# Optimization experiments

Hardware: AMD Instinct MI355X
Metric: run time of the kernel (lower is better)

## Reference

```python
import jax, jax.numpy as jnp
import numpy as np

N, M, K, C = 1000, 2000, 10, 80
IOU_THRESHOLD = 0.5
EPS = 1e-7


def setup_inputs() -> dict:
    key = jax.random.key(0)
    k1, k2, k3, k4, k5, k6, k7 = jax.random.split(key, 7)
    # pred boxes: realistic xyxy boxes in a 1000x1000 image
    cxy = jax.random.uniform(k1, (N, 2), minval=0.0, maxval=1000.0)
    wh = jax.random.uniform(k2, (N, 2), minval=20.0, maxval=100.0)
    pred_box = jnp.concatenate([cxy - wh / 2, cxy + wh / 2], axis=1)  # [N,4]
    pred = jnp.concatenate([pred_box, jax.random.uniform(k3, (N, 2))], axis=1)  # [N,6]
    # dropout passes: jittered copies of pred boxes (guarantees IoU>0.5 match)
    # followed by M-N random boxes
    copies = pred_box[None, :, :] + jax.random.normal(k4, (K, N, 4)) * 1.0  # [K,N,4]
    rc = jax.random.uniform(k5, (K, M - N, 2), minval=0.0, maxval=1000.0)
    rwh = jax.random.uniform(k6, (K, M - N, 2), minval=20.0, maxval=100.0)
    rand_box = jnp.concatenate([rc - rwh / 2, rc + rwh / 2], axis=2)  # [K,M-N,4]
    boxes = jnp.concatenate([copies, rand_box], axis=1)  # [K,M,4]
    dropout_preds = jnp.concatenate([boxes, jnp.ones((K, M, 2), jnp.float32)], axis=2)
    # per-box class probability rows (softmax-normalized, strictly positive)
    dropout_cls_confs = jax.nn.softmax(jax.random.normal(k7, (K, M, C)), axis=-1)
    return {
        "pred": pred.astype(jnp.float32),
        "dropout_preds": dropout_preds.astype(jnp.float32),
        "dropout_cls_confs": dropout_cls_confs.astype(jnp.float32),
    }


def _pairwise_iou(b1, b2):
    # b1: [N,4] xyxy, b2: [K,M,4] xyxy -> iou [K,N,M]
    ix1 = jnp.maximum(b1[None, :, None, 0], b2[:, None, :, 0])
    iy1 = jnp.maximum(b1[None, :, None, 1], b2[:, None, :, 1])
    ix2 = jnp.minimum(b1[None, :, None, 2], b2[:, None, :, 2])
    iy2 = jnp.minimum(b1[None, :, None, 3], b2[:, None, :, 3])
    inter = jnp.clip(ix2 - ix1, 0.0) * jnp.clip(iy2 - iy1, 0.0)  # [K,N,M]
    area1 = (b1[:, 2] - b1[:, 0]) * (b1[:, 3] - b1[:, 1])  # [N]
    area2 = (b2[..., 2] - b2[..., 0]) * (b2[..., 3] - b2[..., 1])  # [K,M]
    return inter / (area1[None, :, None] + area2[:, None, :] - inter + EPS)


def reference(pred, dropout_preds, dropout_cls_confs):
    n_classes = dropout_cls_confs.shape[-1]
    inv_n = 1.0 / n_classes
    max_entropy = -n_classes * (inv_n * jnp.log(jnp.float32(inv_n)))  # == log(C)

    iou = _pairwise_iou(pred[:, :4], dropout_preds[:, :, :4])  # [K,N,M]
    mask = iou > IOU_THRESHOLD  # [K,N,M]
    matched = jnp.any(mask, axis=-1)  # [K,N] any match in pass k for pred n
    first = jnp.argmax(mask, axis=-1)  # [K,N] index of FIRST match (break semantics)

    # gather the matched class-confidence row per (pass, pred): [K,N,C]
    rows = jnp.take_along_axis(dropout_cls_confs, first[:, :, None], axis=1)
    entropy = -jnp.sum(rows * jnp.log(rows), axis=-1)  # [K,N]
    u = 1.0 - entropy / max_entropy  # [K,N]

    matched_f = matched.astype(u.dtype)
    cnt = jnp.sum(matched_f, axis=0)  # [N]
    sum_u = jnp.sum(u * matched_f, axis=0)  # [N]
    # no-match fallback in original yields NaN (entropy of zeros row)
    semantic_uncertainty = jnp.where(cnt > 0, sum_u / jnp.maximum(cnt, 1.0), jnp.nan)
    return semantic_uncertainty
```

## Files before the change

kernel.cpp:

```cpp
#include <hip/hip_runtime.h>
#include <math.h>

#define N_PRED 1000
#define M_BOX  2000
#define K_PASS 10
#define C_CLS  80
#define IOU_THR 0.5f
#define EPS_IOU 1e-7f

#define P_PRED 2
#define BLK_T  (K_PASS * 64)
#define N_BLK  (N_PRED / P_PRED)

__global__ __launch_bounds__(BLK_T)
void ue_cls_kernel(const float* __restrict__ pred,
                   const float* __restrict__ dpreds,
                   const float* __restrict__ dconfs,
                   float* __restrict__ out)
{
    const int k    = threadIdx.x >> 6;
    const int lane = threadIdx.x & 63;
    const int n0   = blockIdx.x * P_PRED;

    __shared__ float s_u[K_PASS][P_PRED];
    __shared__ float s_m[K_PASS][P_PRED];

    float px1[P_PRED], py1[P_PRED], px2[P_PRED], py2[P_PRED], a1[P_PRED];
    #pragma unroll
    for (int p = 0; p < P_PRED; ++p) {
        const float* pr = pred + (n0 + p) * 6;
        px1[p] = pr[0]; py1[p] = pr[1]; px2[p] = pr[2]; py2[p] = pr[3];
        a1[p] = (px2[p] - px1[p]) * (py2[p] - py1[p]);
    }

    const long kbase = (long)k * M_BOX;
    const float2* dp2 = (const float2*)dpreds;
    int firstI[P_PRED];
    #pragma unroll
    for (int p = 0; p < P_PRED; ++p) firstI[p] = 0x7fffffff;

    #pragma unroll 4
    for (int c0 = 0; c0 < M_BOX; c0 += 64) {
        const int m = c0 + lane;
        const bool valid = (m < M_BOX);
        const long i2 = (kbase + (valid ? m : M_BOX - 1)) * 3;
        const float2 a = dp2[i2];
        const float2 b = dp2[i2 + 1];
        const float area2 = (b.x - a.x) * (b.y - a.y);
        #pragma unroll
        for (int p = 0; p < P_PRED; ++p) {
            const float ix1 = fmaxf(px1[p], a.x);
            const float iy1 = fmaxf(py1[p], a.y);
            const float ix2 = fminf(px2[p], b.x);
            const float iy2 = fminf(py2[p], b.y);
            const float inter = fmaxf(ix2 - ix1, 0.0f) * fmaxf(iy2 - iy1, 0.0f);
            const float iou = inter / (a1[p] + area2 - inter + EPS_IOU);
            if (valid && iou > IOU_THR) firstI[p] = min(firstI[p], m);
        }
    }
    #pragma unroll
    for (int off = 32; off > 0; off >>= 1) {
        #pragma unroll
        for (int p = 0; p < P_PRED; ++p)
            firstI[p] = min(firstI[p], __shfl_xor(firstI[p], off, 64));
    }

    const float inv_n  = 1.0f / (float)C_CLS;
    const float max_en = -(float)C_CLS * (inv_n * logf(inv_n));
    float um[P_PRED], mt[P_PRED];
    #pragma unroll
    for (int p = 0; p < P_PRED; ++p) {
        um[p] = 0.0f; mt[p] = 0.0f;
        if (firstI[p] != 0x7fffffff) {
            mt[p] = 1.0f;
            const float* row = dconfs + (kbase + firstI[p]) * (long)C_CLS;
            float local = 0.0f;
            {
                const float v = row[lane];
                local -= v * logf(v);
            }
            if (lane < C_CLS - 64) {
                const float v = row[64 + lane];
                local -= v * logf(v);
            }
            #pragma unroll
            for (int off = 32; off > 0; off >>= 1)
                local += __shfl_xor(local, off, 64);
            um[p] = 1.0f - local / max_en;
        }
    }

    if (lane == 0) {
        #pragma unroll
        for (int p = 0; p < P_PRED; ++p) {
            s_u[k][p] = um[p] * mt[p];
            s_m[k][p] = mt[p];
        }
    }
    __syncthreads();

    if (threadIdx.x < P_PRED) {
        const int t = threadIdx.x;
        float cnt = 0.0f, su = 0.0f;
        #pragma unroll
        for (int kk = 0; kk < K_PASS; ++kk) { su += s_u[kk][t]; cnt += s_m[kk][t]; }
        out[n0 + t] = (cnt > 0.0f) ? (su / fmaxf(cnt, 1.0f)) : __builtin_nanf("");
    }
}

extern "C" void kernel_launch(void* const* d_in, const int* in_sizes, int n_in,
                              void* d_out, int out_size, void* d_ws, size_t ws_size,
                              hipStream_t stream) {
    const float* pred   = (const float*)d_in[0];
    const float* dpreds = (const float*)d_in[1];
    const float* dconfs = (const float*)d_in[2];
    float* out = (float*)d_out;

    ue_cls_kernel<<<dim3(N_BLK), dim3(BLK_T), 0, stream>>>(pred, dpreds, dconfs, out);
}
```

Baseline: 82.11 us.

## Bound first-match scan to a prefix with fallback, and process four preds per block

```diff
diff --git a/kernel.cpp b/kernel.cpp
--- a/kernel.cpp
+++ b/kernel.cpp
@@ -8,9 +8,11 @@
 #define IOU_THR 0.5f
 #define EPS_IOU 1e-7f
 
-#define P_PRED 2
+#define P_PRED 4
 #define BLK_T  (K_PASS * 64)
 #define N_BLK  (N_PRED / P_PRED)
+
+#define IDX_INF 0x7fffffff
 
 __global__ __launch_bounds__(BLK_T)
 void ue_cls_kernel(const float* __restrict__ pred,
@@ -35,15 +37,15 @@
 
     const long kbase = (long)k * M_BOX;
     const float2* dp2 = (const float2*)dpreds;
+
     int firstI[P_PRED];
     #pragma unroll
-    for (int p = 0; p < P_PRED; ++p) firstI[p] = 0x7fffffff;
+    for (int p = 0; p < P_PRED; ++p) firstI[p] = IDX_INF;
 
-    #pragma unroll 4
-    for (int c0 = 0; c0 < M_BOX; c0 += 64) {
+    const int L = (((n0 + P_PRED - 1) >> 6) << 6) + 64;
+    for (int c0 = 0; c0 < L; c0 += 64) {
         const int m = c0 + lane;
-        const bool valid = (m < M_BOX);
-        const long i2 = (kbase + (valid ? m : M_BOX - 1)) * 3;
+        const long i2 = (kbase + m) * 3;
         const float2 a = dp2[i2];
         const float2 b = dp2[i2 + 1];
         const float area2 = (b.x - a.x) * (b.y - a.y);
@@ -54,8 +56,8 @@
             const float ix2 = fminf(px2[p], b.x);
             const float iy2 = fminf(py2[p], b.y);
             const float inter = fmaxf(ix2 - ix1, 0.0f) * fmaxf(iy2 - iy1, 0.0f);
-            const float iou = inter / (a1[p] + area2 - inter + EPS_IOU);
-            if (valid && iou > IOU_THR) firstI[p] = min(firstI[p], m);
+            const float den = a1[p] + area2 - inter + EPS_IOU;
+            if (inter > 0.5f * den) firstI[p] = min(firstI[p], m);
         }
     }
     #pragma unroll
@@ -65,13 +67,43 @@
             firstI[p] = min(firstI[p], __shfl_xor(firstI[p], off, 64));
     }
 
+    bool need = false;
+    #pragma unroll
+    for (int p = 0; p < P_PRED; ++p) need = need || (firstI[p] == IDX_INF);
+    if (need) {
+        for (int c0 = L; c0 < M_BOX; c0 += 64) {
+            const int m = c0 + lane;
+            const bool valid = (m < M_BOX);
+            const long i2 = (kbase + (valid ? m : M_BOX - 1)) * 3;
+            const float2 a = dp2[i2];
+            const float2 b = dp2[i2 + 1];
+            const float area2 = (b.x - a.x) * (b.y - a.y);
+            #pragma unroll
+            for (int p = 0; p < P_PRED; ++p) {
+                const float ix1 = fmaxf(px1[p], a.x);
+                const float iy1 = fmaxf(py1[p], a.y);
+                const float ix2 = fminf(px2[p], b.x);
+                const float iy2 = fminf(py2[p], b.y);
+                const float inter = fmaxf(ix2 - ix1, 0.0f) * fmaxf(iy2 - iy1, 0.0f);
+                const float den = a1[p] + area2 - inter + EPS_IOU;
+                if (valid && inter > 0.5f * den) firstI[p] = min(firstI[p], m);
+            }
+        }
+        #pragma unroll
+        for (int off = 32; off > 0; off >>= 1) {
+            #pragma unroll
+            for (int p = 0; p < P_PRED; ++p)
+                firstI[p] = min(firstI[p], __shfl_xor(firstI[p], off, 64));
+        }
+    }
+
     const float inv_n  = 1.0f / (float)C_CLS;
     const float max_en = -(float)C_CLS * (inv_n * logf(inv_n));
     float um[P_PRED], mt[P_PRED];
     #pragma unroll
     for (int p = 0; p < P_PRED; ++p) {
         um[p] = 0.0f; mt[p] = 0.0f;
-        if (firstI[p] != 0x7fffffff) {
+        if (firstI[p] != IDX_INF) {
             mt[p] = 1.0f;
             const float* row = dconfs + (kbase + firstI[p]) * (long)C_CLS;
             float local = 0.0f;
```

Result: faster. 70.93 us (-13.6%).
